# Kernel optimization log

Measured on AMD Instinct MI355X. Metric: run time of the kernel, lower is better.

## Reference

```python
import jax, jax.numpy as jnp
import numpy as np

N_POINTS = 1_000_000
N_BATCH = 32
C = 128


def setup_inputs() -> dict:
    key = jax.random.key(0)
    k1, k2 = jax.random.split(key)
    x_glob = jax.random.normal(k1, (N_BATCH, C), dtype=jnp.float32)
    batch_idx = jax.random.randint(k2, (N_POINTS,), 0, N_BATCH, dtype=jnp.int32)
    return {"x_glob": x_glob, "batch_idx": batch_idx}


def reference(x_glob, batch_idx):
    # MinkowskiBroadcast: perm_mat @ x_glob where perm_mat is a one-hot
    # [N_points, N_batch] COO matrix -> equivalent to an indexed gather.
    # out[i] = x_glob[batch_idx[i]]
    return jnp.take(x_glob, batch_idx, axis=0)
```

## Files before the change

kernel.cpp:

```cpp
#include <hip/hip_runtime.h>


typedef float v4f __attribute__((ext_vector_type(4)));

__global__ __launch_bounds__(256) void
minkowski_broadcast_kernel(const v4f* __restrict__ xg,
                           const int* __restrict__ bidx,
                           v4f*       __restrict__ out,
                           int n_chunks) {
    int stride = (int)(gridDim.x * blockDim.x);
    for (int g = (int)(blockIdx.x * blockDim.x + threadIdx.x);
         g < n_chunks; g += stride) {
        int p  = g >> 5;
        int c4 = g & 31;
        int b  = bidx[p];
        v4f v  = xg[(b << 5) + c4];
        out[g] = v;
    }
}

extern "C" void kernel_launch(void* const* d_in, const int* in_sizes, int n_in,
                              void* d_out, int out_size, void* d_ws, size_t ws_size,
                              hipStream_t stream) {
    const v4f* xg   = (const v4f*)d_in[0];
    const int* bidx = (const int*)d_in[1];
    v4f*       out  = (v4f*)d_out;

    const int n_chunks = out_size / 4;

    const int block = 256;
    const int grid  = 2048;
    minkowski_broadcast_kernel<<<grid, block, 0, stream>>>(xg, bidx, out, n_chunks);
}
```

Measured before the change: 536.6 us.

## Stage x_glob in LDS and software-pipeline batched index prefetch

Each block copies the whole 32x128 x_glob table (16 KB) into shared memory and then serves the gathers from LDS instead of global/L2. The grid-stride loop is restructured into batches of 8 iterations, with the batch indices for the next batch prefetched while the current batch's stores are issued. This aims to hide index-load latency and remove dependent global gather loads. In exchange, each block now spends time loading 16 KB into LDS and uses more registers.

```diff
diff --git a/kernel.cpp b/kernel.cpp
--- a/kernel.cpp
+++ b/kernel.cpp
@@ -2,20 +2,44 @@
 
 
 typedef float v4f __attribute__((ext_vector_type(4)));
+
+#define BATCH 8
 
 __global__ __launch_bounds__(256) void
 minkowski_broadcast_kernel(const v4f* __restrict__ xg,
                            const int* __restrict__ bidx,
                            v4f*       __restrict__ out,
                            int n_chunks) {
-    int stride = (int)(gridDim.x * blockDim.x);
-    for (int g = (int)(blockIdx.x * blockDim.x + threadIdx.x);
-         g < n_chunks; g += stride) {
-        int p  = g >> 5;
-        int c4 = g & 31;
-        int b  = bidx[p];
-        v4f v  = xg[(b << 5) + c4];
-        out[g] = v;
+    __shared__ v4f lds_xg[32 * 32];
+    for (int i = threadIdx.x; i < 32 * 32; i += 256)
+        lds_xg[i] = xg[i];
+    __syncthreads();
+
+    const int tid    = (int)(blockIdx.x * blockDim.x + threadIdx.x);
+    const int stride = (int)(gridDim.x * blockDim.x);
+    int b[BATCH];
+#pragma unroll
+    for (int k = 0; k < BATCH; ++k) {
+        int g = tid + k * stride;
+        b[k] = (g < n_chunks) ? bidx[g >> 5] : 0;
+    }
+
+    for (int base = tid; base < n_chunks; base += BATCH * stride) {
+        int bn[BATCH];
+        const int nbase = base + BATCH * stride;
+#pragma unroll
+        for (int k = 0; k < BATCH; ++k) {
+            int g = nbase + k * stride;
+            bn[k] = (g < n_chunks) ? bidx[g >> 5] : 0;
+        }
+#pragma unroll
+        for (int k = 0; k < BATCH; ++k) {
+            int g = base + k * stride;
+            if (g < n_chunks)
+                out[g] = lds_xg[(b[k] << 5) + (g & 31)];
+        }
+#pragma unroll
+        for (int k = 0; k < BATCH; ++k) b[k] = bn[k];
     }
 }
 
```

Measured after the change: 516.1 us. 1.04x faster.
